# Kernel optimization log

Measured on AMD Instinct MI355X. Metric: run time of the kernel, lower is better.

The kernel has to match this reference:

```python
import jax, jax.numpy as jnp
import numpy as np

NUM_NEG_INDICES_FOR_LOSS = 5
NUM_NEG_PAIRS = 64
C, H, W = 256, 512, 512


def setup_inputs() -> dict:
    key = jax.random.key(0)
    k1, k2, k3 = jax.random.split(key, 3)
    feats1 = jax.random.normal(k1, (1, C, H, W), dtype=jnp.float32)
    feats2 = jax.random.normal(k2, (1, C, H, W), dtype=jnp.float32)
    positive_pairs = jax.random.randint(k3, (1, NUM_NEG_PAIRS, 2), 0, H * W, dtype=jnp.int64)
    return {"feats1": feats1, "feats2": feats2, "positive_pairs": positive_pairs}


def reference(feats1, feats2, positive_pairs):
    # feats*: [1, C, H, W]; positive_pairs: [1, P, 2] with P == NUM_NEG_PAIRS
    b, c, h, w = feats1.shape
    f1 = feats1.reshape(c, -1)  # [C, HW] (valid because b == 1, matching torch view)
    f2 = feats2.reshape(c, -1)  # [C, HW]
    idx = positive_pairs[0, :, 0]  # [P] anchor pixel indices into flattened image 1
    sel = f1[:, idx].T             # [P, C] anchor descriptors
    # Squared L2 distance from each anchor to every pixel of image 2 via the
    # ||a||^2 + ||b||^2 - 2 a.b expansion (one [P,C]x[C,HW] GEMM).
    d = (jnp.sum(sel * sel, axis=1, keepdims=True)
         + jnp.sum(f2 * f2, axis=0)[None, :]
         - 2.0 * (sel @ f2))       # [P, HW]
    d = jax.nn.relu(d)             # matches functional.relu (also clamps fp error)
    # Hardest negatives = smallest distances. NOTE: the torch neighborhood-mask
    # exclusion compares a float distance VALUE against an int index array, so
    # it is dead code in practice -> effective math is plain top-k smallest.
    neg_vals, _ = jax.lax.top_k(-d, NUM_NEG_INDICES_FOR_LOSS)  # [P, 5]
    per_pair = jnp.mean(-neg_vals, axis=1)                     # [P]
    return jnp.sum(per_pair) / NUM_NEG_PAIRS
```

## Files before the change

kernel.cpp:

```cpp
#include <hip/hip_runtime.h>
#include <hip/hip_bf16.h>

#define HW_   262144
#define C_    256
#define NP_   64
#define NBLK_ 1024
#define SENT  3.0e38f

typedef __attribute__((ext_vector_type(8))) __bf16 bf16x8;
typedef __attribute__((ext_vector_type(4))) float f32x4;

__device__ __forceinline__ void top5_insert(float (&t)[5], float v) {
  if (v < t[4]) {
    t[4] = v;
    if (t[4] < t[3]) { float x = t[3]; t[3] = t[4]; t[4] = x; }
    if (t[3] < t[2]) { float x = t[2]; t[2] = t[3]; t[3] = x; }
    if (t[2] < t[1]) { float x = t[1]; t[1] = t[2]; t[2] = x; }
    if (t[1] < t[0]) { float x = t[0]; t[0] = t[1]; t[1] = x; }
  }
}

__global__ void gather_sel_kernel(const float* __restrict__ f1,
                                  const void* __restrict__ pairs,
                                  unsigned short* __restrict__ selb,
                                  float* __restrict__ n_p) {
  __shared__ float red[256];
  __shared__ int sidx;
  const int p = blockIdx.x, t = threadIdx.x;
  if (t == 0) {
    const long long* ll = (const long long*)pairs;
    const int* ii = (const int*)pairs;
    bool is64 = true;
    for (int k = 0; k < 8; ++k) {
      long long v = ll[k];
      if (v < 0 || v >= (long long)HW_) is64 = false;
    }
    sidx = is64 ? (int)ll[2 * p] : ii[2 * p];
  }
  __syncthreads();
  const int idx = sidx;
  float v = f1[(size_t)t * HW_ + idx];
  __bf16 b = (__bf16)v;
  selb[p * 256 + t] = __builtin_bit_cast(unsigned short, b);
  red[t] = v * v;
  __syncthreads();
  for (int s = 128; s > 0; s >>= 1) {
    if (t < s) red[t] += red[t + s];
    __syncthreads();
  }
  if (t == 0) n_p[p] = red[0];
}

__global__ __launch_bounds__(512, 4) void dist_topk_kernel(
    const float* __restrict__ f2, const unsigned short* __restrict__ selb,
    const float* __restrict__ n_p, float* __restrict__ cand) {
  __shared__ float smem[64 * 256];
  char* smemB = (char*)smem;
  const int tid = threadIdx.x;
  const int w = tid >> 6, lane = tid & 63;
  const int m_l = lane & 15, kq = lane >> 4;
  const int j0 = blockIdx.x * 256;

  {
    const uint4* src = (const uint4*)selb;
#pragma unroll
    for (int i = 0; i < 4; ++i) {
      const int idx = i * 512 + tid;
      const int m = idx >> 5;
      unsigned off = (unsigned)(idx * 16) ^ ((m & 7) << 4);
      *(uint4*)(smemB + off) = src[idx];
    }
  }
  __syncthreads();

  const unsigned colbase = (unsigned)(j0 + w * 32 + m_l);
  const unsigned rowbase = (unsigned)(kq * 8) * HW_;

  f32x4 acc[4][2];
#pragma unroll
  for (int mt = 0; mt < 4; ++mt)
#pragma unroll
    for (int nt = 0; nt < 2; ++nt) acc[mt][nt] = (f32x4){0.f, 0.f, 0.f, 0.f};
  float njp[2] = {0.f, 0.f};

  float b0[16], b1[16], b2[16];
#define LOADB(BUF, T)                                                          \
  _Pragma("unroll") for (int nt = 0; nt < 2; ++nt)                             \
  _Pragma("unroll") for (int e = 0; e < 8; ++e)                                \
      BUF[nt * 8 + e] =                                                        \
          f2[rowbase + colbase + (unsigned)(((T) * 32 + e) * HW_ + nt * 16)];

  LOADB(b0, 0)
  LOADB(b1, 1)

#define STEP(CUR, NXT, T, PF)                                                   \
  {                                                                             \
    if (PF) { LOADB(NXT, (T) + 2) }                                             \
    bf16x8 afr[4];                                                              \
    _Pragma("unroll") for (int mt = 0; mt < 4; ++mt) {                          \
      unsigned offA =                                                           \
          (unsigned)((mt * 16 + m_l) * 512 + kq * 16 + (T) * 64) ^              \
          ((m_l & 7) << 4);                                                     \
      afr[mt] = *(const bf16x8*)(smemB + offA);                                 \
    }                                                                           \
    bf16x8 bfr[2];                                                              \
    _Pragma("unroll") for (int nt = 0; nt < 2; ++nt) {                          \
      _Pragma("unroll") for (int e = 0; e < 8; ++e) {                           \
        float v = CUR[nt * 8 + e];                                              \
        njp[nt] = fmaf(v, v, njp[nt]);                                          \
        bfr[nt][e] = (__bf16)v;                                                 \
      }                                                                         \
    }                                                                           \
    _Pragma("unroll") for (int mt = 0; mt < 4; ++mt)                            \
      _Pragma("unroll") for (int nt = 0; nt < 2; ++nt)                          \
        acc[mt][nt] = __builtin_amdgcn_mfma_f32_16x16x32_bf16(                  \
            afr[mt], bfr[nt], acc[mt][nt], 0, 0, 0);                            \
  }

  STEP(b0, b2, 0, 1) STEP(b1, b0, 1, 1) STEP(b2, b1, 2, 1) STEP(b0, b2, 3, 1)
  STEP(b1, b0, 4, 1) STEP(b2, b1, 5, 1) STEP(b0, b2, 6, 0) STEP(b1, b0, 7, 0)
#undef STEP
#undef LOADB

  float njc[2];
#pragma unroll
  for (int nt = 0; nt < 2; ++nt) {
    float v = njp[nt];
    v += __shfl_xor(v, 16);
    v += __shfl_xor(v, 32);
    njc[nt] = v;
  }

  __syncthreads();

#pragma unroll
  for (int mt = 0; mt < 4; ++mt) {
#pragma unroll
    for (int r = 0; r < 4; ++r) {
      const int pair = mt * 16 + kq * 4 + r;
      const float np = n_p[pair];
#pragma unroll
      for (int nt = 0; nt < 2; ++nt) {
        const int col = w * 32 + nt * 16 + m_l;
        float d = np + njc[nt] - 2.0f * acc[mt][nt][r];
        smem[pair * 256 + (col ^ (pair & 31))] = fmaxf(d, 0.0f);
      }
    }
  }
  __syncthreads();

  const int pp = tid & 63, q = tid >> 6;
  float t5[5] = {SENT, SENT, SENT, SENT, SENT};
#pragma unroll 4
  for (int i = 0; i < 32; ++i) {
    const int col = q * 32 + i;
    float v = smem[pp * 256 + (col ^ (pp & 31))];
    top5_insert(t5, v);
  }
  __syncthreads();
#pragma unroll
  for (int k = 0; k < 5; ++k) smem[tid * 5 + k] = t5[k];
  __syncthreads();
  if (tid < 64) {
    float m5[5] = {SENT, SENT, SENT, SENT, SENT};
    for (int g = 0; g < 8; ++g)
#pragma unroll
      for (int k = 0; k < 5; ++k) top5_insert(m5, smem[(g * 64 + tid) * 5 + k]);
    float* cc = cand + (size_t)blockIdx.x * (NP_ * 5) + tid * 5;
#pragma unroll
    for (int k = 0; k < 5; ++k) cc[k] = m5[k];
  }
}

__global__ void topk_reduce_kernel(const float* __restrict__ cand,
                                   float* __restrict__ mean5) {
  __shared__ float lds[256 * 5];
  const int p = blockIdx.x, tid = threadIdx.x;
  float t5[5] = {SENT, SENT, SENT, SENT, SENT};
  for (int b = tid; b < NBLK_; b += 256) {
    const float* cc = cand + (size_t)b * (NP_ * 5) + p * 5;
#pragma unroll
    for (int k = 0; k < 5; ++k) top5_insert(t5, cc[k]);
  }
#pragma unroll
  for (int k = 0; k < 5; ++k) lds[tid * 5 + k] = t5[k];
  __syncthreads();
  float m2[5] = {SENT, SENT, SENT, SENT, SENT};
  if (tid < 32) {
    for (int t2 = tid * 8; t2 < tid * 8 + 8; ++t2)
#pragma unroll
      for (int k = 0; k < 5; ++k) top5_insert(m2, lds[t2 * 5 + k]);
  }
  __syncthreads();
  if (tid < 32) {
#pragma unroll
    for (int k = 0; k < 5; ++k) lds[tid * 5 + k] = m2[k];
  }
  __syncthreads();
  if (tid == 0) {
    float f[5] = {SENT, SENT, SENT, SENT, SENT};
    for (int t2 = 0; t2 < 32; ++t2)
#pragma unroll
      for (int k = 0; k < 5; ++k) top5_insert(f, lds[t2 * 5 + k]);
    mean5[p] = (f[0] + f[1] + f[2] + f[3] + f[4]) * 0.2f;
  }
}

__global__ void final_sum_kernel(const float* __restrict__ mean5,
                                 float* __restrict__ out) {
  const int tid = threadIdx.x;
  float v = mean5[tid];
  for (int off = 32; off > 0; off >>= 1) v += __shfl_down(v, off);
  if (tid == 0) out[0] = v * (1.0f / 64.0f);
}

extern "C" void kernel_launch(void* const* d_in, const int* in_sizes, int n_in,
                              void* d_out, int out_size, void* d_ws, size_t ws_size,
                              hipStream_t stream) {
  const float* f1 = (const float*)d_in[0];
  const float* f2 = (const float*)d_in[1];
  const void* pairs = d_in[2];
  float* out = (float*)d_out;
  float* ws = (float*)d_ws;

  float*          n_p   = ws;
  unsigned short* selb  = (unsigned short*)(ws + 64);
  float*          cand  = ws + 64 + 8192;
  float*          mean5 = ws + 64 + 8192 + 327680;

  gather_sel_kernel<<<NP_, 256, 0, stream>>>(f1, pairs, selb, n_p);
  dist_topk_kernel<<<NBLK_, 512, 0, stream>>>(f2, selb, n_p, cand);
  topk_reduce_kernel<<<NP_, 256, 0, stream>>>(cand, mean5);
  final_sum_kernel<<<1, 64, 0, stream>>>(mean5, out);
}
```

Baseline: 82.77 us.

## Stream f2 tiles via async global-to-LDS loads with triple buffering

Replaces the per-thread register prefetch of f2 with global_load_lds direct-to-LDS 16-byte copies into a three-stage swizzled LDS ring, synchronised with explicit vmcnt waits. Blocks shrink to 256 threads covering 128 columns, so the grid doubles to 2048 and the candidate buffer grows. The aim is deeper memory-level parallelism and less register pressure on this bandwidth-bound GEMM. In exchange it uses 80KB of LDS per block, which limits occupancy, and doubles the partial top-k work in the reduction kernel.

```diff
diff --git a/kernel.cpp b/kernel.cpp
--- a/kernel.cpp
+++ b/kernel.cpp
@@ -4,11 +4,19 @@
 #define HW_   262144
 #define C_    256
 #define NP_   64
-#define NBLK_ 1024
+#define BCOLS 128
+#define NBLK_ 2048
 #define SENT  3.0e38f
 
 typedef __attribute__((ext_vector_type(8))) __bf16 bf16x8;
 typedef __attribute__((ext_vector_type(4))) float f32x4;
+
+typedef const __attribute__((address_space(1))) void* gas_ptr;
+typedef __attribute__((address_space(3))) void* las_ptr;
+
+__device__ __forceinline__ void gload16(const void* g, void* l) {
+  __builtin_amdgcn_global_load_lds((gas_ptr)g, (las_ptr)l, 16, 0, 0);
+}
 
 __device__ __forceinline__ void top5_insert(float (&t)[5], float v) {
   if (v < t[4]) {
@@ -51,21 +59,21 @@
   if (t == 0) n_p[p] = red[0];
 }
 
-__global__ __launch_bounds__(512, 4) void dist_topk_kernel(
+__global__ __launch_bounds__(256, 2) void dist_topk_kernel(
     const float* __restrict__ f2, const unsigned short* __restrict__ selb,
     const float* __restrict__ n_p, float* __restrict__ cand) {
-  __shared__ float smem[64 * 256];
-  char* smemB = (char*)smem;
+  __shared__ __align__(16) char smemB[81920];
+  float* smemF = (float*)smemB;
   const int tid = threadIdx.x;
   const int w = tid >> 6, lane = tid & 63;
   const int m_l = lane & 15, kq = lane >> 4;
-  const int j0 = blockIdx.x * 256;
+  const int j0 = blockIdx.x * BCOLS;
 
   {
     const uint4* src = (const uint4*)selb;
 #pragma unroll
-    for (int i = 0; i < 4; ++i) {
-      const int idx = i * 512 + tid;
+    for (int i = 0; i < 8; ++i) {
+      const int idx = i * 256 + tid;
       const int m = idx >> 5;
       unsigned off = (unsigned)(idx * 16) ^ ((m & 7) << 4);
       *(uint4*)(smemB + off) = src[idx];
@@ -73,8 +81,12 @@
   }
   __syncthreads();
 
-  const unsigned colbase = (unsigned)(j0 + w * 32 + m_l);
-  const unsigned rowbase = (unsigned)(kq * 8) * HW_;
+#define ISSUE(T, BUF)                                                          \
+  _Pragma("unroll") for (int ii = 0; ii < 4; ++ii) {                           \
+    const float* gg = f2 + (size_t)((T) * 32 + ii * 8 + (lane >> 3)) * HW_ +   \
+                      j0 + (8 * w + ((lane & 7) ^ ii)) * 4;                    \
+    gload16(gg, smemB + 32768 + (BUF) * 16384 + w * 4096 + ii * 1024);         \
+  }
 
   f32x4 acc[4][2];
 #pragma unroll
@@ -83,30 +95,23 @@
     for (int nt = 0; nt < 2; ++nt) acc[mt][nt] = (f32x4){0.f, 0.f, 0.f, 0.f};
   float njp[2] = {0.f, 0.f};
 
-  float b0[16], b1[16], b2[16];
-#define LOADB(BUF, T)                                                          \
-  _Pragma("unroll") for (int nt = 0; nt < 2; ++nt)                             \
-  _Pragma("unroll") for (int e = 0; e < 8; ++e)                                \
-      BUF[nt * 8 + e] =                                                        \
-          f2[rowbase + colbase + (unsigned)(((T) * 32 + e) * HW_ + nt * 16)];
-
-  LOADB(b0, 0)
-  LOADB(b1, 1)
-
-#define STEP(CUR, NXT, T, PF)                                                   \
+#define STEP(T, BUF, WAITN)                                                     \
   {                                                                             \
-    if (PF) { LOADB(NXT, (T) + 2) }                                             \
+    asm volatile("s_waitcnt vmcnt(" WAITN ")" ::: "memory");                    \
+    const char* Bs = smemB + 32768 + (BUF) * 16384 + w * 4096;                  \
     bf16x8 afr[4];                                                              \
     _Pragma("unroll") for (int mt = 0; mt < 4; ++mt) {                          \
-      unsigned offA =                                                           \
-          (unsigned)((mt * 16 + m_l) * 512 + kq * 16 + (T) * 64) ^              \
-          ((m_l & 7) << 4);                                                     \
+      unsigned offA = (unsigned)((mt * 16 + m_l) * 512 + kq * 16 + (T) * 64) ^  \
+                      ((m_l & 7) << 4);                                         \
       afr[mt] = *(const bf16x8*)(smemB + offA);                                 \
     }                                                                           \
     bf16x8 bfr[2];                                                              \
     _Pragma("unroll") for (int nt = 0; nt < 2; ++nt) {                          \
+      const int c = m_l + 16 * nt;                                              \
       _Pragma("unroll") for (int e = 0; e < 8; ++e) {                           \
-        float v = CUR[nt * 8 + e];                                              \
+        const int row = kq * 8 + e;                                             \
+        float v = *(const float*)(Bs + row * 128 + (((c >> 2) ^ kq) * 16) +     \
+                                  (c & 3) * 4);                                 \
         njp[nt] = fmaf(v, v, njp[nt]);                                          \
         bfr[nt][e] = (__bf16)v;                                                 \
       }                                                                         \
@@ -117,10 +122,17 @@
             afr[mt], bfr[nt], acc[mt][nt], 0, 0, 0);                            \
   }
 
-  STEP(b0, b2, 0, 1) STEP(b1, b0, 1, 1) STEP(b2, b1, 2, 1) STEP(b0, b2, 3, 1)
-  STEP(b1, b0, 4, 1) STEP(b2, b1, 5, 1) STEP(b0, b2, 6, 0) STEP(b1, b0, 7, 0)
+  ISSUE(0, 0) ISSUE(1, 1) ISSUE(2, 2)
+  STEP(0, 0, "8") ISSUE(3, 0)
+  STEP(1, 1, "8") ISSUE(4, 1)
+  STEP(2, 2, "8") ISSUE(5, 2)
+  STEP(3, 0, "8") ISSUE(6, 0)
+  STEP(4, 1, "8") ISSUE(7, 1)
+  STEP(5, 2, "8")
+  STEP(6, 0, "4")
+  STEP(7, 1, "0")
 #undef STEP
-#undef LOADB
+#undef ISSUE
 
   float njc[2];
 #pragma unroll
@@ -143,7 +155,7 @@
       for (int nt = 0; nt < 2; ++nt) {
         const int col = w * 32 + nt * 16 + m_l;
         float d = np + njc[nt] - 2.0f * acc[mt][nt][r];
-        smem[pair * 256 + (col ^ (pair & 31))] = fmaxf(d, 0.0f);
+        smemF[pair * 128 + (col ^ (pair & 31))] = fmaxf(d, 0.0f);
       }
     }
   }
@@ -154,18 +166,18 @@
 #pragma unroll 4
   for (int i = 0; i < 32; ++i) {
     const int col = q * 32 + i;
-    float v = smem[pp * 256 + (col ^ (pp & 31))];
+    float v = smemF[pp * 128 + (col ^ (pp & 31))];
     top5_insert(t5, v);
   }
   __syncthreads();
 #pragma unroll
-  for (int k = 0; k < 5; ++k) smem[tid * 5 + k] = t5[k];
+  for (int k = 0; k < 5; ++k) smemF[tid * 5 + k] = t5[k];
   __syncthreads();
   if (tid < 64) {
     float m5[5] = {SENT, SENT, SENT, SENT, SENT};
-    for (int g = 0; g < 8; ++g)
-#pragma unroll
-      for (int k = 0; k < 5; ++k) top5_insert(m5, smem[(g * 64 + tid) * 5 + k]);
+    for (int g = 0; g < 4; ++g)
+#pragma unroll
+      for (int k = 0; k < 5; ++k) top5_insert(m5, smemF[(g * 64 + tid) * 5 + k]);
     float* cc = cand + (size_t)blockIdx.x * (NP_ * 5) + tid * 5;
 #pragma unroll
     for (int k = 0; k < 5; ++k) cc[k] = m5[k];
@@ -226,10 +238,10 @@
   float*          n_p   = ws;
   unsigned short* selb  = (unsigned short*)(ws + 64);
   float*          cand  = ws + 64 + 8192;
-  float*          mean5 = ws + 64 + 8192 + 327680;
+  float*          mean5 = ws + 64 + 8192 + 655360;
 
   gather_sel_kernel<<<NP_, 256, 0, stream>>>(f1, pairs, selb, n_p);
-  dist_topk_kernel<<<NBLK_, 512, 0, stream>>>(f2, selb, n_p, cand);
+  dist_topk_kernel<<<NBLK_, 256, 0, stream>>>(f2, selb, n_p, cand);
   topk_reduce_kernel<<<NP_, 256, 0, stream>>>(cand, mean5);
   final_sum_kernel<<<1, 64, 0, stream>>>(mean5, out);
 }
```

New measurement: 94.41 us. 1.14x slower.
